# Kernel optimization log

Hardware: AMD Instinct MI355X
Metric: run time of the kernel (lower is better)

Reference implementation:

```python
import jax, jax.numpy as jnp
import numpy as np

T = 65536      # total tokens (flattened ragged batch)
H = 1024       # hidden size
B = 64         # number of segments (documents)
L = 2          # num_labels
EPS = 1e-12    # electra layer_norm_eps


def setup_inputs() -> dict:
    key = jax.random.key(0)
    k1, k2, k3, k4, k5, k6 = jax.random.split(key, 6)
    # ragged segment ids: sorted random ids in [0, B) covering all segments
    rng = np.random.default_rng(0)
    cuts = np.sort(rng.choice(np.arange(1, T), size=B - 1, replace=False))
    lengths = np.diff(np.concatenate([[0], cuts, [T]]))  # B positive lengths summing to T
    segment_ids = jnp.asarray(np.repeat(np.arange(B), lengths), dtype=jnp.int32)
    return {
        "sequence_attention_embeddings": jax.random.normal(k1, (T, H), dtype=jnp.float32),
        "sequence_embeddings": jax.random.normal(k2, (T, H), dtype=jnp.float32),
        "W_dense": jax.random.normal(k3, (H, H), dtype=jnp.float32) / np.sqrt(H),
        "b_dense": jnp.zeros((H,), dtype=jnp.float32),
        "gamma": jnp.ones((H,), dtype=jnp.float32),
        "beta": jnp.zeros((H,), dtype=jnp.float32),
        "W_out": jax.random.normal(k4, (H, L), dtype=jnp.float32) / np.sqrt(H),
        "b_out": jnp.zeros((L,), dtype=jnp.float32),
        "segment_ids": segment_ids,
    }


def reference(sequence_attention_embeddings, sequence_embeddings, W_dense, b_dense,
              gamma, beta, W_out, b_out, segment_ids):
    # dense projection on flattened tokens [T, H]
    h = sequence_attention_embeddings @ W_dense + b_dense
    # dropout is identity in eval mode
    # residual + LayerNorm
    h = h + sequence_embeddings
    mu = jnp.mean(h, axis=-1, keepdims=True)
    var = jnp.mean(jnp.square(h - mu), axis=-1, keepdims=True)
    h = (h - mu) / jnp.sqrt(var + EPS) * gamma + beta
    # ragged split + per-segment mean == fused segment mean
    sums = jax.ops.segment_sum(h, segment_ids, num_segments=B)          # [B, H]
    counts = jax.ops.segment_sum(jnp.ones((h.shape[0],), h.dtype), segment_ids, num_segments=B)
    agg = sums / counts[:, None]
    # final projection to logits [B, L]
    return agg @ W_out + b_out
```

## Files before the change

kernel.cpp:

```cpp
#include <hip/hip_runtime.h>

#define T_TOK 65536
#define HDIM  1024
#define NSEG  64

typedef _Float16 half8  __attribute__((ext_vector_type(8)));
typedef float    f32x2  __attribute__((ext_vector_type(2)));
typedef float    f32x4  __attribute__((ext_vector_type(4)));
typedef float    f32x16 __attribute__((ext_vector_type(16)));

#define WP_OFF   0ull
#define U0_OFF   2097152ull
#define U1_OFF   (U0_OFF + 4096ull)
#define CON_OFF  (U1_OFF + 4096ull)
#define ACC_OFF  (CON_OFF + 64ull)
#define CNT_OFF  (ACC_OFF + 512ull)

__global__ void prep_kernel(const float* __restrict__ gamma, const float* __restrict__ beta,
                            const float* __restrict__ wout, const int* __restrict__ segids,
                            float* __restrict__ u0, float* __restrict__ u1,
                            float* __restrict__ consts, float* __restrict__ segacc,
                            int* __restrict__ counts) {
    __shared__ int   starts[65];
    __shared__ float cacc[4];
    int tid = threadIdx.x;
    if (tid < 128) segacc[tid] = 0.f;
    if (tid < 4)   cacc[tid]   = 0.f;
    if (tid == 0) { starts[0] = 0; starts[64] = T_TOK; }
    __syncthreads();

    float g  = gamma[tid], be = beta[tid];
    float w0 = wout[2 * tid], w1 = wout[2 * tid + 1];
    float a0 = g * w0, a1 = g * w1;
    u0[tid] = a0; u1[tid] = a1;
    float v[4] = {a0, a1, be * w0, be * w1};
#pragma unroll
    for (int q = 0; q < 4; ++q) {
        float x = v[q];
#pragma unroll
        for (int off = 32; off > 0; off >>= 1) x += __shfl_down(x, off, 64);
        if ((tid & 63) == 0) atomicAdd(&cacc[q], x);
    }
    for (int i = tid; i < T_TOK - 1; i += 1024) {
        int s0 = segids[i], s1 = segids[i + 1];
        if (s1 != s0) starts[s1] = i + 1;
    }
    __syncthreads();
    if (tid < 64) counts[tid] = starts[tid + 1] - starts[tid];
    if (tid < 4)  consts[tid] = cacc[tid];
}

__global__ void wpack_kernel(const float* __restrict__ W, _Float16* __restrict__ Wp) {
    __shared__ float tile[64][65];
    int bx = blockIdx.x & 15;
    int by = blockIdx.x >> 4;
    int c0 = bx * 64, k0 = by * 64;
    int t  = threadIdx.x;
    int kk = t >> 6, cc = t & 63;
#pragma unroll
    for (int i = 0; i < 16; ++i) {
        int kl = kk * 16 + i;
        tile[kl][cc] = W[(size_t)(k0 + kl) * HDIM + c0 + cc];
    }
    __syncthreads();
    int cti  = t >> 7;
    int ksgi = (t >> 5) & 3;
    int ln   = t & 31;
    int ct   = (c0 >> 5) + cti;
    int ksg  = (k0 >> 4) + ksgi;
#pragma unroll
    for (int lh = 0; lh < 2; ++lh) {
        int l = lh * 32 + ln;
        half8 v;
#pragma unroll
        for (int j = 0; j < 8; ++j)
            v[j] = (_Float16)tile[ksgi * 16 + lh * 8 + j][cti * 32 + ln];
        *(half8*)(Wp + ((size_t)(ct * 64 + ksg) * 64 + l) * 8) = v;
    }
}

#define A_LDS 33280

__global__ __launch_bounds__(1024, 4) void gemm_kernel(
    const float* __restrict__ A, const float* __restrict__ R,
    const float* __restrict__ bdense, const _Float16* __restrict__ Wp,
    const float* __restrict__ u0g, const float* __restrict__ u1g,
    const float* __restrict__ consts, const int* __restrict__ segids,
    float* __restrict__ segacc) {
    __shared__ __align__(16) char smem[A_LDS + 512 + 256];
    int tid  = threadIdx.x;
    int lane = tid & 63, wave = tid >> 6;
    int ln = lane & 31, lh = lane >> 5;
    int rowBase = blockIdx.x * 64;
    int colW    = wave * 64;

    f32x16 acc[2][2];
#pragma unroll
    for (int tr = 0; tr < 2; ++tr)
#pragma unroll
        for (int tc = 0; tc < 2; ++tc)
#pragma unroll
            for (int i = 0; i < 16; ++i) acc[tr][tc][i] = 0.f;

    const _Float16* bp[2];
#pragma unroll
    for (int tc = 0; tc < 2; ++tc)
        bp[tc] = Wp + ((size_t)(wave * 2 + tc) * 64 * 64 + lane) * 8;

    int khalf = tid & 31;
    int mloc0 = tid >> 5;

    for (int kq = 0; kq < 4; ++kq) {
        __syncthreads();
#pragma unroll
        for (int i = 0; i < 2; ++i) {
            int mloc = mloc0 + i * 32;
            const float* src = A + (size_t)(rowBase + mloc) * HDIM + kq * 256 + khalf * 8;
            f32x4 a0 = *(const f32x4*)src;
            f32x4 a1 = *(const f32x4*)(src + 4);
            half8 s;
            s[0] = (_Float16)a0[0]; s[1] = (_Float16)a0[1];
            s[2] = (_Float16)a0[2]; s[3] = (_Float16)a0[3];
            s[4] = (_Float16)a1[0]; s[5] = (_Float16)a1[1];
            s[6] = (_Float16)a1[2]; s[7] = (_Float16)a1[3];
            *(half8*)(smem + khalf * 1040 + mloc * 16) = s;
        }
        __syncthreads();
#pragma unroll
        for (int ks = 0; ks < 16; ++ks) {
            int ksg = kq * 16 + ks;
            half8 afr[2], bfr[2];
#pragma unroll
            for (int tc = 0; tc < 2; ++tc)
                bfr[tc] = *(const half8*)(bp[tc] + (size_t)ksg * 512);
#pragma unroll
            for (int tr = 0; tr < 2; ++tr)
                afr[tr] = *(const half8*)(smem + (ks * 2 + lh) * 1040 + (tr * 32 + ln) * 16);
#pragma unroll
            for (int tr = 0; tr < 2; ++tr)
#pragma unroll
                for (int tc = 0; tc < 2; ++tc)
                    acc[tr][tc] = __builtin_amdgcn_mfma_f32_32x32x16_f16(
                        afr[tr], bfr[tc], acc[tr][tc], 0, 0, 0);
        }
    }

    __syncthreads();
    float* red  = (float*)smem;
#pragma unroll
    for (int i = 0; i < 8; ++i) red[tid + i * 1024] = 0.f;
    float* sval = (float*)(smem + A_LDS);
    int*   sseg = (int*)(smem + A_LDS + 512);
    __syncthreads();

    float bv[2], u0v[2], u1v[2];
#pragma unroll
    for (int tc = 0; tc < 2; ++tc) {
        int c = colW + tc * 32 + ln;
        bv[tc] = bdense[c]; u0v[tc] = u0g[c]; u1v[tc] = u1g[c];
    }
#pragma unroll
    for (int tr = 0; tr < 2; ++tr)
#pragma unroll
        for (int reg = 0; reg < 16; ++reg) {
            int rIT   = (reg & 3) + 8 * (reg >> 2) + 4 * lh;
            int row64 = tr * 32 + rIT;
            size_t grow = (size_t)(rowBase + row64);
            float s1 = 0.f, s2 = 0.f, p0 = 0.f, p1 = 0.f;
#pragma unroll
            for (int tc = 0; tc < 2; ++tc) {
                float h = acc[tr][tc][reg] + bv[tc] + R[grow * HDIM + colW + tc * 32 + ln];
                s1 += h; s2 += h * h; p0 += h * u0v[tc]; p1 += h * u1v[tc];
            }
            atomicAdd(&red[row64 * 32 + ln], s1);
            atomicAdd(&red[2048 + row64 * 32 + ln], s2);
            atomicAdd(&red[4096 + row64 * 32 + ln], p0);
            atomicAdd(&red[6144 + row64 * 32 + ln], p1);
        }
    __syncthreads();
    {
        int r = tid >> 4, i = tid & 15;
        int j = (i + r) & 15;
        f32x2 v0 = *(f32x2*)&red[r * 32 + 2 * j];
        f32x2 v1 = *(f32x2*)&red[2048 + r * 32 + 2 * j];
        f32x2 v2 = *(f32x2*)&red[4096 + r * 32 + 2 * j];
        f32x2 v3 = *(f32x2*)&red[6144 + r * 32 + 2 * j];
        float s1 = v0[0] + v0[1], s2 = v1[0] + v1[1];
        float p0 = v2[0] + v2[1], p1 = v3[0] + v3[1];
#pragma unroll
        for (int off = 1; off < 16; off <<= 1) {
            s1 += __shfl_xor(s1, off, 64);
            s2 += __shfl_xor(s2, off, 64);
            p0 += __shfl_xor(p0, off, 64);
            p1 += __shfl_xor(p1, off, 64);
        }
        if (i == 0) {
            float mu  = s1 * (1.f / 1024.f);
            float var = s2 * (1.f / 1024.f) - mu * mu;
            float rsd = rsqrtf(var + 1e-12f);
            sval[r * 2]     = rsd * (p0 - mu * consts[0]) + consts[2];
            sval[r * 2 + 1] = rsd * (p1 - mu * consts[1]) + consts[3];
            sseg[r] = segids[rowBase + r];
        }
    }
    __syncthreads();
    if (tid < 64) {
        int s = sseg[tid];
        if (tid == 63 || sseg[tid + 1] != s) {
            float a0 = 0.f, a1 = 0.f;
            int rr = tid;
            while (rr >= 0 && sseg[rr] == s) { a0 += sval[rr * 2]; a1 += sval[rr * 2 + 1]; --rr; }
            atomicAdd(&segacc[s * 2],     a0);
            atomicAdd(&segacc[s * 2 + 1], a1);
        }
    }
}

__global__ void finalize_kernel(const float* __restrict__ segacc, const int* __restrict__ counts,
                                const float* __restrict__ bout, float* __restrict__ out) {
    int t = threadIdx.x;
    if (t < 128) {
        int s = t >> 1, l = t & 1;
        out[t] = segacc[t] / (float)counts[s] + bout[l];
    }
}

extern "C" void kernel_launch(void* const* d_in, const int* in_sizes, int n_in,
                              void* d_out, int out_size, void* d_ws, size_t ws_size,
                              hipStream_t stream) {
    const float* A      = (const float*)d_in[0];
    const float* R      = (const float*)d_in[1];
    const float* Wd     = (const float*)d_in[2];
    const float* bdense = (const float*)d_in[3];
    const float* gamma  = (const float*)d_in[4];
    const float* beta   = (const float*)d_in[5];
    const float* wout   = (const float*)d_in[6];
    const float* bout   = (const float*)d_in[7];
    const int*   segids = (const int*)d_in[8];
    float* out = (float*)d_out;

    char* ws = (char*)d_ws;
    _Float16* Wp  = (_Float16*)(ws + WP_OFF);
    float* u0     = (float*)(ws + U0_OFF);
    float* u1     = (float*)(ws + U1_OFF);
    float* consts = (float*)(ws + CON_OFF);
    float* segacc = (float*)(ws + ACC_OFF);
    int*   counts = (int*)(ws + CNT_OFF);

    prep_kernel<<<1, 1024, 0, stream>>>(gamma, beta, wout, segids, u0, u1, consts, segacc, counts);
    wpack_kernel<<<256, 256, 0, stream>>>(Wd, Wp);
    gemm_kernel<<<1024, 1024, 0, stream>>>(A, R, bdense, Wp, u0, u1, consts, segids, segacc);
    finalize_kernel<<<1, 128, 0, stream>>>(segacc, counts, bout, out);
}
```

Before: 1.241 ms.

## Retile GEMM to 128x128 blocks with LDS-staged weights and split row-reduction kernel

The GEMM moves from 64-row blocks spanning all 1024 columns with 1024 threads to 128x128 output tiles with 256 threads and a K chunk of 64. Weight tiles are now staged into LDS with global_load_lds instead of being read per wave from global memory. Because each block now covers only part of a row, per-row partial LayerNorm statistics are atomically accumulated into a global rowfunc buffer, and a new logits kernel finishes normalization and segment sums. This brings memsets, an extra kernel and global atomics, and each block now re-reads and re-converts its A rows from fp32 eight times (once per column block), adding A traffic.

New measurement: 1.370 ms. 10.4% more time.

```diff
diff --git a/kernel.cpp b/kernel.cpp
--- a/kernel.cpp
+++ b/kernel.cpp
@@ -3,9 +3,11 @@
 #define T_TOK 65536
 #define HDIM  1024
 #define NSEG  64
+#define BM 128
+#define BN 128
+#define BK 64
 
 typedef _Float16 half8  __attribute__((ext_vector_type(8)));
-typedef float    f32x2  __attribute__((ext_vector_type(2)));
 typedef float    f32x4  __attribute__((ext_vector_type(4)));
 typedef float    f32x16 __attribute__((ext_vector_type(16)));
 
@@ -15,17 +17,22 @@
 #define CON_OFF  (U1_OFF + 4096ull)
 #define ACC_OFF  (CON_OFF + 64ull)
 #define CNT_OFF  (ACC_OFF + 512ull)
+#define RF_OFF   (CNT_OFF + 256ull)
+
+__device__ __forceinline__ void gload_lds16(const void* g, void* l) {
+    __builtin_amdgcn_global_load_lds(
+        (const __attribute__((address_space(1))) unsigned int*)g,
+        (__attribute__((address_space(3))) unsigned int*)l, 16, 0, 0);
+}
 
 __global__ void prep_kernel(const float* __restrict__ gamma, const float* __restrict__ beta,
                             const float* __restrict__ wout, const int* __restrict__ segids,
                             float* __restrict__ u0, float* __restrict__ u1,
-                            float* __restrict__ consts, float* __restrict__ segacc,
-                            int* __restrict__ counts) {
+                            float* __restrict__ consts, int* __restrict__ counts) {
     __shared__ int   starts[65];
     __shared__ float cacc[4];
     int tid = threadIdx.x;
-    if (tid < 128) segacc[tid] = 0.f;
-    if (tid < 4)   cacc[tid]   = 0.f;
+    if (tid < 4)   cacc[tid] = 0.f;
     if (tid == 0) { starts[0] = 0; starts[64] = T_TOK; }
     __syncthreads();
 
@@ -79,20 +86,22 @@
     }
 }
 
-#define A_LDS 33280
-
-__global__ __launch_bounds__(1024, 4) void gemm_kernel(
+__global__ __launch_bounds__(256, 4) void gemm_kernel(
     const float* __restrict__ A, const float* __restrict__ R,
     const float* __restrict__ bdense, const _Float16* __restrict__ Wp,
     const float* __restrict__ u0g, const float* __restrict__ u1g,
-    const float* __restrict__ consts, const int* __restrict__ segids,
-    float* __restrict__ segacc) {
-    __shared__ __align__(16) char smem[A_LDS + 512 + 256];
+    float* __restrict__ rowfunc) {
+    __shared__ __align__(16) _Float16 lds[BM * BK + BN * BK];
+    _Float16* aS = lds;
+    _Float16* bS = lds + BM * BK;
+
     int tid  = threadIdx.x;
     int lane = tid & 63, wave = tid >> 6;
+    int wr = wave >> 1, wc = wave & 1;
     int ln = lane & 31, lh = lane >> 5;
-    int rowBase = blockIdx.x * 64;
-    int colW    = wave * 64;
+    int rowBase = (blockIdx.x >> 3) * BM;
+    int colg    = blockIdx.x & 7;
+    int ct0     = colg * 4;
 
     f32x16 acc[2][2];
 #pragma unroll
@@ -102,40 +111,48 @@
 #pragma unroll
             for (int i = 0; i < 16; ++i) acc[tr][tc][i] = 0.f;
 
-    const _Float16* bp[2];
-#pragma unroll
-    for (int tc = 0; tc < 2; ++tc)
-        bp[tc] = Wp + ((size_t)(wave * 2 + tc) * 64 * 64 + lane) * 8;
-
-    int khalf = tid & 31;
-    int mloc0 = tid >> 5;
-
-    for (int kq = 0; kq < 4; ++kq) {
+    int sr = tid & 127;
+    int sh = tid >> 7;
+    const float* aSrc = A + (size_t)(rowBase + sr) * HDIM + sh * 32;
+    int aDstBase[4];
+#pragma unroll
+    for (int j = 0; j < 4; ++j) {
+        int ksgi = sh * 2 + (j >> 1), lhf = j & 1;
+        aDstBase[j] = ((ksgi * 4 + (sr >> 5)) * 64 + (sr & 31) + 32 * lhf) * 8;
+    }
+
+    for (int kc = 0; kc < 16; ++kc) {
         __syncthreads();
 #pragma unroll
-        for (int i = 0; i < 2; ++i) {
-            int mloc = mloc0 + i * 32;
-            const float* src = A + (size_t)(rowBase + mloc) * HDIM + kq * 256 + khalf * 8;
-            f32x4 a0 = *(const f32x4*)src;
-            f32x4 a1 = *(const f32x4*)(src + 4);
-            half8 s;
-            s[0] = (_Float16)a0[0]; s[1] = (_Float16)a0[1];
-            s[2] = (_Float16)a0[2]; s[3] = (_Float16)a0[3];
-            s[4] = (_Float16)a1[0]; s[5] = (_Float16)a1[1];
-            s[6] = (_Float16)a1[2]; s[7] = (_Float16)a1[3];
-            *(half8*)(smem + khalf * 1040 + mloc * 16) = s;
+        for (int i = 0; i < 4; ++i) {
+            int idx  = wave * 4 + i;
+            int cti  = idx >> 2, ksgi = idx & 3;
+            int chunk = (ct0 + cti) * 64 + kc * 4 + ksgi;
+            gload_lds16(Wp + (size_t)chunk * 512 + lane * 8,
+                        bS + (size_t)(cti * 4 + ksgi) * 512);
+        }
+        const float* s = aSrc + kc * 64;
+#pragma unroll
+        for (int j = 0; j < 4; ++j) {
+            f32x4 a0 = *(const f32x4*)(s + j * 8);
+            f32x4 a1 = *(const f32x4*)(s + j * 8 + 4);
+            half8 hh;
+            hh[0] = (_Float16)a0[0]; hh[1] = (_Float16)a0[1];
+            hh[2] = (_Float16)a0[2]; hh[3] = (_Float16)a0[3];
+            hh[4] = (_Float16)a1[0]; hh[5] = (_Float16)a1[1];
+            hh[6] = (_Float16)a1[2]; hh[7] = (_Float16)a1[3];
+            *(half8*)(aS + aDstBase[j]) = hh;
         }
         __syncthreads();
 #pragma unroll
-        for (int ks = 0; ks < 16; ++ks) {
-            int ksg = kq * 16 + ks;
+        for (int ks = 0; ks < 4; ++ks) {
             half8 afr[2], bfr[2];
 #pragma unroll
+            for (int tr = 0; tr < 2; ++tr)
+                afr[tr] = *(const half8*)(aS + ((ks * 4 + wr * 2 + tr) * 64 + lane) * 8);
+#pragma unroll
             for (int tc = 0; tc < 2; ++tc)
-                bfr[tc] = *(const half8*)(bp[tc] + (size_t)ksg * 512);
-#pragma unroll
-            for (int tr = 0; tr < 2; ++tr)
-                afr[tr] = *(const half8*)(smem + (ks * 2 + lh) * 1040 + (tr * 32 + ln) * 16);
+                bfr[tc] = *(const half8*)(bS + (((wc * 2 + tc) * 4 + ks) * 64 + lane) * 8);
 #pragma unroll
             for (int tr = 0; tr < 2; ++tr)
 #pragma unroll
@@ -146,73 +163,72 @@
     }
 
     __syncthreads();
-    float* red  = (float*)smem;
-#pragma unroll
-    for (int i = 0; i < 8; ++i) red[tid + i * 1024] = 0.f;
-    float* sval = (float*)(smem + A_LDS);
-    int*   sseg = (int*)(smem + A_LDS + 512);
+    float* red = (float*)lds;
+#pragma unroll
+    for (int i = 0; i < 8; ++i)
+        *(f32x4*)(red + (tid + i * 256) * 4) = (f32x4){0.f, 0.f, 0.f, 0.f};
     __syncthreads();
 
     float bv[2], u0v[2], u1v[2];
 #pragma unroll
     for (int tc = 0; tc < 2; ++tc) {
-        int c = colW + tc * 32 + ln;
+        int c = colg * 128 + wc * 64 + tc * 32 + ln;
         bv[tc] = bdense[c]; u0v[tc] = u0g[c]; u1v[tc] = u1g[c];
     }
+    int sl = ln & 15;
 #pragma unroll
     for (int tr = 0; tr < 2; ++tr)
 #pragma unroll
         for (int reg = 0; reg < 16; ++reg) {
-            int rIT   = (reg & 3) + 8 * (reg >> 2) + 4 * lh;
-            int row64 = tr * 32 + rIT;
-            size_t grow = (size_t)(rowBase + row64);
+            int row128 = wr * 64 + tr * 32 + ((reg & 3) + 8 * (reg >> 2) + 4 * lh);
+            const float* rrow = R + (size_t)(rowBase + row128) * HDIM
+                                  + colg * 128 + wc * 64 + ln;
             float s1 = 0.f, s2 = 0.f, p0 = 0.f, p1 = 0.f;
 #pragma unroll
             for (int tc = 0; tc < 2; ++tc) {
-                float h = acc[tr][tc][reg] + bv[tc] + R[grow * HDIM + colW + tc * 32 + ln];
+                float h = acc[tr][tc][reg] + bv[tc] + rrow[tc * 32];
                 s1 += h; s2 += h * h; p0 += h * u0v[tc]; p1 += h * u1v[tc];
             }
-            atomicAdd(&red[row64 * 32 + ln], s1);
-            atomicAdd(&red[2048 + row64 * 32 + ln], s2);
-            atomicAdd(&red[4096 + row64 * 32 + ln], p0);
-            atomicAdd(&red[6144 + row64 * 32 + ln], p1);
-        }
-    __syncthreads();
-    {
-        int r = tid >> 4, i = tid & 15;
-        int j = (i + r) & 15;
-        f32x2 v0 = *(f32x2*)&red[r * 32 + 2 * j];
-        f32x2 v1 = *(f32x2*)&red[2048 + r * 32 + 2 * j];
-        f32x2 v2 = *(f32x2*)&red[4096 + r * 32 + 2 * j];
-        f32x2 v3 = *(f32x2*)&red[6144 + r * 32 + 2 * j];
-        float s1 = v0[0] + v0[1], s2 = v1[0] + v1[1];
-        float p0 = v2[0] + v2[1], p1 = v3[0] + v3[1];
-#pragma unroll
-        for (int off = 1; off < 16; off <<= 1) {
-            s1 += __shfl_xor(s1, off, 64);
-            s2 += __shfl_xor(s2, off, 64);
-            p0 += __shfl_xor(p0, off, 64);
-            p1 += __shfl_xor(p1, off, 64);
-        }
-        if (i == 0) {
-            float mu  = s1 * (1.f / 1024.f);
-            float var = s2 * (1.f / 1024.f) - mu * mu;
-            float rsd = rsqrtf(var + 1e-12f);
-            sval[r * 2]     = rsd * (p0 - mu * consts[0]) + consts[2];
-            sval[r * 2 + 1] = rsd * (p1 - mu * consts[1]) + consts[3];
-            sseg[r] = segids[rowBase + r];
-        }
-    }
-    __syncthreads();
-    if (tid < 64) {
-        int s = sseg[tid];
-        if (tid == 63 || sseg[tid + 1] != s) {
-            float a0 = 0.f, a1 = 0.f;
-            int rr = tid;
-            while (rr >= 0 && sseg[rr] == s) { a0 += sval[rr * 2]; a1 += sval[rr * 2 + 1]; --rr; }
-            atomicAdd(&segacc[s * 2],     a0);
-            atomicAdd(&segacc[s * 2 + 1], a1);
-        }
+            atomicAdd(&red[(0 * 128 + row128) * 16 + sl], s1);
+            atomicAdd(&red[(1 * 128 + row128) * 16 + sl], s2);
+            atomicAdd(&red[(2 * 128 + row128) * 16 + sl], p0);
+            atomicAdd(&red[(3 * 128 + row128) * 16 + sl], p1);
+        }
+    __syncthreads();
+#pragma unroll
+    for (int s = 0; s < 2; ++s) {
+        int slot = tid + s * 256;
+        int q = slot >> 7, row = slot & 127;
+        const float* p = red + (size_t)(q * 128 + row) * 16;
+        f32x4 v0 = *(const f32x4*)p,       v1 = *(const f32x4*)(p + 4);
+        f32x4 v2 = *(const f32x4*)(p + 8), v3 = *(const f32x4*)(p + 12);
+        float sum = (v0[0] + v0[1] + v0[2] + v0[3]) + (v1[0] + v1[1] + v1[2] + v1[3])
+                  + (v2[0] + v2[1] + v2[2] + v2[3]) + (v3[0] + v3[1] + v3[2] + v3[3]);
+        atomicAdd(&rowfunc[(size_t)(rowBase + row) * 4 + q], sum);
+    }
+}
+
+__global__ void logits_kernel(const float* __restrict__ rowfunc, const float* __restrict__ consts,
+                              const int* __restrict__ segids, float* __restrict__ segacc) {
+    __shared__ float sval[256][2];
+    __shared__ int   sseg[256];
+    int t   = threadIdx.x;
+    int row = blockIdx.x * 256 + t;
+    f32x4 f = *(const f32x4*)(rowfunc + (size_t)row * 4);
+    float mu  = f[0] * (1.f / 1024.f);
+    float var = f[1] * (1.f / 1024.f) - mu * mu;
+    float rsd = rsqrtf(var + 1e-12f);
+    sval[t][0] = rsd * (f[2] - mu * consts[0]) + consts[2];
+    sval[t][1] = rsd * (f[3] - mu * consts[1]) + consts[3];
+    sseg[t] = segids[row];
+    __syncthreads();
+    int sg = sseg[t];
+    if (t == 255 || sseg[t + 1] != sg) {
+        float a0 = 0.f, a1 = 0.f;
+        int rr = t;
+        while (rr >= 0 && sseg[rr] == sg) { a0 += sval[rr][0]; a1 += sval[rr][1]; --rr; }
+        atomicAdd(&segacc[sg * 2],     a0);
+        atomicAdd(&segacc[sg * 2 + 1], a1);
     }
 }
 
@@ -240,15 +256,19 @@
     float* out = (float*)d_out;
 
     char* ws = (char*)d_ws;
-    _Float16* Wp  = (_Float16*)(ws + WP_OFF);
-    float* u0     = (float*)(ws + U0_OFF);
-    float* u1     = (float*)(ws + U1_OFF);
-    float* consts = (float*)(ws + CON_OFF);
-    float* segacc = (float*)(ws + ACC_OFF);
-    int*   counts = (int*)(ws + CNT_OFF);
-
-    prep_kernel<<<1, 1024, 0, stream>>>(gamma, beta, wout, segids, u0, u1, consts, segacc, counts);
+    _Float16* Wp   = (_Float16*)(ws + WP_OFF);
+    float* u0      = (float*)(ws + U0_OFF);
+    float* u1      = (float*)(ws + U1_OFF);
+    float* consts  = (float*)(ws + CON_OFF);
+    float* segacc  = (float*)(ws + ACC_OFF);
+    int*   counts  = (int*)(ws + CNT_OFF);
+    float* rowfunc = (float*)(ws + RF_OFF);
+
+    hipMemsetAsync(segacc, 0, 512, stream);
+    hipMemsetAsync(rowfunc, 0, (size_t)T_TOK * 4 * sizeof(float), stream);
+    prep_kernel<<<1, 1024, 0, stream>>>(gamma, beta, wout, segids, u0, u1, consts, counts);
     wpack_kernel<<<256, 256, 0, stream>>>(Wd, Wp);
-    gemm_kernel<<<1024, 1024, 0, stream>>>(A, R, bdense, Wp, u0, u1, consts, segids, segacc);
+    gemm_kernel<<<4096, 256, 0, stream>>>(A, R, bdense, Wp, u0, u1, rowfunc);
+    logits_kernel<<<T_TOK / 256, 256, 0, stream>>>(rowfunc, consts, segids, segacc);
     finalize_kernel<<<1, 128, 0, stream>>>(segacc, counts, bout, out);
 }
```
